# Kernel tuning notes

Hardware: AMD Instinct MI355X
Metric: run time of the kernel (lower is better)

Reference implementation:

```python
import jax, jax.numpy as jnp
import numpy as np

B, N, D, WIN = 2, 4096, 256, 16


def setup_inputs() -> dict:
    key = jax.random.key(0)
    ks = jax.random.split(key, 10)
    def lin(k, o, i):
        return 0.02 * jax.random.normal(k, (o, i), jnp.float32)
    W = N // WIN
    return {
        "x": 0.5 * jax.random.normal(ks[0], (B, N, D), jnp.float32),
        "embed_qk": jax.random.normal(ks[1], (3, B, W, WIN, WIN, 3), jnp.float32),
        "act_proj_w": lin(ks[2], D, D), "act_proj_b": jnp.zeros((D,), jnp.float32),
        "proj_ln_g": jnp.ones((D,), jnp.float32), "proj_ln_b": jnp.zeros((D,), jnp.float32),
        "conv_w": lin(ks[3], D, D), "conv_b": jnp.zeros((D,), jnp.float32),
        "q_w": lin(ks[4], D, D), "q_b": jnp.zeros((D,), jnp.float32),
        "k_w": lin(ks[5], D, D), "k_b": jnp.zeros((D,), jnp.float32),
        "p_w": lin(ks[6], 1, 3), "p_b": jnp.zeros((1,), jnp.float32),
        "lin_w": lin(ks[7], D, D), "lin_b": jnp.zeros((D,), jnp.float32),
        "norm_g": jnp.ones((D,), jnp.float32), "norm_b": jnp.zeros((D,), jnp.float32),
    }


def _ln(x, g, b, eps=1e-5):
    m = x.mean(-1, keepdims=True)
    v = ((x - m) ** 2).mean(-1, keepdims=True)
    return (x - m) * jax.lax.rsqrt(v + eps) * g + b


def reference(x, embed_qk, act_proj_w, act_proj_b, proj_ln_g, proj_ln_b,
              conv_w, conv_b, q_w, q_b, k_w, k_b, p_w, p_b,
              lin_w, lin_b, norm_g, norm_b):
    # MSMAttentionLayer: gated residual path
    act_res = jax.nn.silu(x @ act_proj_w.T + act_proj_b)          # (B,N,C)
    h = _ln(x, proj_ln_g, proj_ln_b)
    h = jax.nn.silu(h @ conv_w.T + conv_b)                        # 1x1 conv == per-token linear

    # MSMLMultiHeadAttention, stage=1 (window 4x4=16); N % 16 == 0 so add_row_num = 0
    q = jax.nn.elu(h @ q_w.T + q_b) + 1.0
    k = jax.nn.elu(h @ k_w.T + k_b) + 1.0
    v = h
    Bn, Nn, C = h.shape
    Wn = Nn // WIN
    q_win = q.reshape(Bn, Wn, WIN, C)
    k_win = k.reshape(Bn, Wn, WIN, C)
    v_win = v.reshape(Bn, Wn, WIN, C)
    # learned relative-position bias: Linear(3,1) on embed_qk[stage]
    p = (embed_qk[1] @ p_w.T + p_b)[..., 0]
    # second elu+1 feature map (applied on top of q/k which are already elu+1)
    phi_q = jax.nn.elu(q_win) + 1.0
    phi_k = jax.nn.elu(k_win) + 1.0
    # linear-attention style KV aggregation: reduces over windows w
    KV = jnp.einsum('bwmc,bwmd->bmcd', phi_k, v_win)
    att = jnp.einsum('bwnc,bmcd->bwnmd', phi_q, KV) + p[..., None]
    attn_out = att.reshape(Bn, -1, C)[:, :Nn, :]                  # (B,N,C)

    hid = (attn_out * act_res) @ lin_w.T + lin_b
    return _ln(hid + h, norm_g, norm_b)
```

## Files before the change

### kernel.cpp

```cpp
#include <hip/hip_runtime.h>


#define DIM 256
#define NTOK 4096

typedef __attribute__((ext_vector_type(8))) short short8;
typedef __attribute__((ext_vector_type(4))) short short4v;
typedef __attribute__((ext_vector_type(4))) float f32x4;

__device__ __forceinline__ float silu_f(float z) { return z / (1.f + __expf(-z)); }
__device__ __forceinline__ float elu2_f(float z) { return z > 0.f ? z + 2.f : __expf(z) + 1.f; }

__device__ __forceinline__ short f2bf(float f) {
    union { float f; unsigned u; } v; v.f = f;
    unsigned r = v.u + 0x7fffu + ((v.u >> 16) & 1u);
    return (short)(r >> 16);
}
__device__ __forceinline__ float bf2f(short s) {
    union { unsigned u; float f; } v; v.u = ((unsigned)(unsigned short)s) << 16;
    return v.f;
}
__device__ __forceinline__ short8 cvt8(const float* src) {
    const float4 a = *(const float4*)src;
    const float4 c = *(const float4*)(src + 4);
    short8 s;
    s[0] = f2bf(a.x); s[1] = f2bf(a.y); s[2] = f2bf(a.z); s[3] = f2bf(a.w);
    s[4] = f2bf(c.x); s[5] = f2bf(c.y); s[6] = f2bf(c.z); s[7] = f2bf(c.w);
    return s;
}
__device__ __forceinline__ void cast_chunk(const float* __restrict__ src, short* __restrict__ dst,
                                           int chunk, int tid) {
    const int base = chunk * 8192 + tid * 32;
    #pragma unroll
    for (int j = 0; j < 4; ++j)
        *(short8*)(dst + base + j * 8) = cvt8(src + base + j * 8);
}

__global__ __launch_bounds__(256) void fused_dual(
        const float* __restrict__ XF,
        const float* __restrict__ W0f, const float* __restrict__ b0, short* __restrict__ Y0,
        const float* __restrict__ W1f, const float* __restrict__ b1, short* __restrict__ Y1,
        const float* __restrict__ G, const float* __restrict__ Bt,
        const float* __restrict__ Wkf, short* __restrict__ WKB,
        const float* __restrict__ Wqf, short* __restrict__ WQB) {
    const int tid = threadIdx.x;
    if (blockIdx.x >= 64) {
        if (blockIdx.y == 0 && blockIdx.z == 0) {
            const int which = blockIdx.x - 64;
            if (which < 8) cast_chunk(Wkf, WKB, which, tid);
            else cast_chunk(Wqf, WQB, which - 8, tid);
        }
        return;
    }
    __shared__ __align__(16) short Xs[2][128 * 72];
    __shared__ __align__(16) short Ws[2][64 * 72];
    __shared__ float stats[128][2];
    const int zz = blockIdx.z;
    const float* Wf = zz ? W1f : W0f;
    const float* bias = zz ? b1 : b0;
    short* Y = zz ? Y1 : Y0;
    const int wv = tid >> 6, l = tid & 63;
    const int lr = l & 15, lk = l >> 4;
    const int r0 = blockIdx.x * 128, c0 = blockIdx.y * 64;
    const int wm = (wv >> 1) * 64, wn = (wv & 1) * 32;
    const int sr = tid >> 3, sc = (tid & 7) * 8;

    if (zz) {
        const int prow = tid >> 1, phalf = tid & 1;
        const float* src = XF + (size_t)(r0 + prow) * DIM + phalf * 128;
        float a1 = 0.f, a2 = 0.f;
        #pragma unroll 8
        for (int j = 0; j < 32; ++j) {
            const float4 v = *(const float4*)(src + j * 4);
            a1 += v.x + v.y + v.z + v.w;
            a2 += v.x * v.x + v.y * v.y + v.z * v.z + v.w * v.w;
        }
        a1 += __shfl_xor(a1, 1);
        a2 += __shfl_xor(a2, 1);
        if (!phalf) {
            const float mm = a1 * (1.f / DIM);
            stats[prow][0] = mm;
            stats[prow][1] = rsqrtf(a2 * (1.f / DIM) - mm * mm + 1e-5f);
        }
        __syncthreads();
    }

    f32x4 acc[4][2];
    #pragma unroll
    for (int i = 0; i < 4; ++i)
        #pragma unroll
        for (int j = 0; j < 2; ++j) acc[i][j] = (f32x4){0.f, 0.f, 0.f, 0.f};

    float4 xa[4][2], wa[2][2];
    #pragma unroll
    for (int p = 0; p < 4; ++p) {
        const float* src = XF + (size_t)(r0 + sr + p * 32) * DIM + sc;
        xa[p][0] = *(const float4*)src;
        xa[p][1] = *(const float4*)(src + 4);
    }
    #pragma unroll
    for (int p = 0; p < 2; ++p) {
        const float* src = Wf + (size_t)(c0 + sr + p * 32) * DIM + sc;
        wa[p][0] = *(const float4*)src;
        wa[p][1] = *(const float4*)(src + 4);
    }

    int buf = 0;
    for (int s = 0; s < 4; ++s) {
        const int kt = s * 64;
        if (zz) {
            const float4 g1 = *(const float4*)(G + kt + sc);
            const float4 g2 = *(const float4*)(G + kt + sc + 4);
            const float4 t1 = *(const float4*)(Bt + kt + sc);
            const float4 t2 = *(const float4*)(Bt + kt + sc + 4);
            const float gv[8] = {g1.x, g1.y, g1.z, g1.w, g2.x, g2.y, g2.z, g2.w};
            const float bv[8] = {t1.x, t1.y, t1.z, t1.w, t2.x, t2.y, t2.z, t2.w};
            #pragma unroll
            for (int p = 0; p < 4; ++p) {
                const int row = sr + p * 32;
                const float mm = stats[row][0], rs = stats[row][1];
                const float v[8] = {xa[p][0].x, xa[p][0].y, xa[p][0].z, xa[p][0].w,
                                    xa[p][1].x, xa[p][1].y, xa[p][1].z, xa[p][1].w};
                short8 sS;
                #pragma unroll
                for (int j = 0; j < 8; ++j) sS[j] = f2bf((v[j] - mm) * rs * gv[j] + bv[j]);
                *(short8*)&Xs[buf][row * 72 + sc] = sS;
            }
        } else {
            #pragma unroll
            for (int p = 0; p < 4; ++p) {
                const int row = sr + p * 32;
                const float v[8] = {xa[p][0].x, xa[p][0].y, xa[p][0].z, xa[p][0].w,
                                    xa[p][1].x, xa[p][1].y, xa[p][1].z, xa[p][1].w};
                short8 sS;
                #pragma unroll
                for (int j = 0; j < 8; ++j) sS[j] = f2bf(v[j]);
                *(short8*)&Xs[buf][row * 72 + sc] = sS;
            }
        }
        #pragma unroll
        for (int p = 0; p < 2; ++p) {
            const int row = sr + p * 32;
            const float v[8] = {wa[p][0].x, wa[p][0].y, wa[p][0].z, wa[p][0].w,
                                wa[p][1].x, wa[p][1].y, wa[p][1].z, wa[p][1].w};
            short8 sS;
            #pragma unroll
            for (int j = 0; j < 8; ++j) sS[j] = f2bf(v[j]);
            *(short8*)&Ws[buf][row * 72 + sc] = sS;
        }
        __syncthreads();
        if (s < 3) {
            const int ktn = kt + 64;
            #pragma unroll
            for (int p = 0; p < 4; ++p) {
                const float* src = XF + (size_t)(r0 + sr + p * 32) * DIM + ktn + sc;
                xa[p][0] = *(const float4*)src;
                xa[p][1] = *(const float4*)(src + 4);
            }
            #pragma unroll
            for (int p = 0; p < 2; ++p) {
                const float* src = Wf + (size_t)(c0 + sr + p * 32) * DIM + ktn + sc;
                wa[p][0] = *(const float4*)src;
                wa[p][1] = *(const float4*)(src + 4);
            }
        }
        #pragma unroll
        for (int kc = 0; kc < 2; ++kc) {
            short8 af[4], bfr[2];
            #pragma unroll
            for (int mi = 0; mi < 4; ++mi)
                af[mi] = *(const short8*)&Xs[buf][(wm + mi * 16 + lr) * 72 + kc * 32 + lk * 8];
            #pragma unroll
            for (int ni = 0; ni < 2; ++ni)
                bfr[ni] = *(const short8*)&Ws[buf][(wn + ni * 16 + lr) * 72 + kc * 32 + lk * 8];
            #pragma unroll
            for (int mi = 0; mi < 4; ++mi)
                #pragma unroll
                for (int ni = 0; ni < 2; ++ni)
                    acc[mi][ni] = __builtin_amdgcn_mfma_f32_16x16x32_bf16(af[mi], bfr[ni], acc[mi][ni], 0, 0, 0);
        }
        buf ^= 1;
    }
    #pragma unroll
    for (int mi = 0; mi < 4; ++mi)
        #pragma unroll
        for (int ni = 0; ni < 2; ++ni) {
            const int c = c0 + wn + ni * 16 + lr;
            const float bv2 = bias[c];
            #pragma unroll
            for (int i = 0; i < 4; ++i) {
                const int r = r0 + wm + mi * 16 + lk * 4 + i;
                Y[(size_t)r * DIM + c] = f2bf(silu_f(acc[mi][ni][i] + bv2));
            }
        }
}

__global__ __launch_bounds__(256) void gemm_kq(
        const short* __restrict__ H, const short* __restrict__ WKB, const float* __restrict__ bk, short* __restrict__ PK,
        const short* __restrict__ WQB, const float* __restrict__ bq, short* __restrict__ PQ) {
    __shared__ __align__(16) short Xs[2][128 * 72];
    __shared__ __align__(16) short Ws[2][64 * 72];
    const int bx = blockIdx.x;
    const bool isq = bx >= 64;
    const short* W = isq ? WQB : WKB;
    const float* bias = isq ? bq : bk;
    short* Y = isq ? PQ : PK;
    const int r0 = (isq ? bx - 64 : bx) * 128;
    const int c0 = blockIdx.y * 64;
    const int tid = threadIdx.x;
    const int wv = tid >> 6, l = tid & 63;
    const int lr = l & 15, lk = l >> 4;
    const int wm = (wv >> 1) * 64, wn = (wv & 1) * 32;
    const int sr = tid >> 3, sc = (tid & 7) * 8;

    int growA[4];
    #pragma unroll
    for (int p = 0; p < 4; ++p) {
        int grow = r0 + sr + p * 32;
        if (isq) grow = ((grow >> 8) << 12) + (grow & 255);
        growA[p] = grow;
    }

    f32x4 acc[4][2];
    #pragma unroll
    for (int i = 0; i < 4; ++i)
        #pragma unroll
        for (int j = 0; j < 2; ++j) acc[i][j] = (f32x4){0.f, 0.f, 0.f, 0.f};

    short8 xa[4], wa[2];
    #pragma unroll
    for (int p = 0; p < 4; ++p)
        xa[p] = *(const short8*)(H + (size_t)growA[p] * DIM + sc);
    #pragma unroll
    for (int p = 0; p < 2; ++p)
        wa[p] = *(const short8*)(W + (size_t)(c0 + sr + p * 32) * DIM + sc);

    int buf = 0;
    for (int s = 0; s < 4; ++s) {
        #pragma unroll
        for (int p = 0; p < 4; ++p)
            *(short8*)&Xs[buf][(sr + p * 32) * 72 + sc] = xa[p];
        #pragma unroll
        for (int p = 0; p < 2; ++p)
            *(short8*)&Ws[buf][(sr + p * 32) * 72 + sc] = wa[p];
        __syncthreads();
        if (s < 3) {
            const int ktn = (s + 1) * 64;
            #pragma unroll
            for (int p = 0; p < 4; ++p)
                xa[p] = *(const short8*)(H + (size_t)growA[p] * DIM + ktn + sc);
            #pragma unroll
            for (int p = 0; p < 2; ++p)
                wa[p] = *(const short8*)(W + (size_t)(c0 + sr + p * 32) * DIM + ktn + sc);
        }
        #pragma unroll
        for (int kc = 0; kc < 2; ++kc) {
            short8 af[4], bfr[2];
            #pragma unroll
            for (int mi = 0; mi < 4; ++mi)
                af[mi] = *(const short8*)&Xs[buf][(wm + mi * 16 + lr) * 72 + kc * 32 + lk * 8];
            #pragma unroll
            for (int ni = 0; ni < 2; ++ni)
                bfr[ni] = *(const short8*)&Ws[buf][(wn + ni * 16 + lr) * 72 + kc * 32 + lk * 8];
            #pragma unroll
            for (int mi = 0; mi < 4; ++mi)
                #pragma unroll
                for (int ni = 0; ni < 2; ++ni)
                    acc[mi][ni] = __builtin_amdgcn_mfma_f32_16x16x32_bf16(af[mi], bfr[ni], acc[mi][ni], 0, 0, 0);
        }
        buf ^= 1;
    }
    #pragma unroll
    for (int mi = 0; mi < 4; ++mi)
        #pragma unroll
        for (int ni = 0; ni < 2; ++ni) {
            const int c = c0 + wn + ni * 16 + lr;
            const float bv = bias[c];
            #pragma unroll
            for (int i = 0; i < 4; ++i) {
                const int r = r0 + wm + mi * 16 + lk * 4 + i;
                Y[(size_t)r * DIM + c] = f2bf(elu2_f(acc[mi][ni][i] + bv));
            }
        }
}

__global__ __launch_bounds__(256) void kv_mfma(const short* __restrict__ HB, const short* __restrict__ PK,
                                               short* __restrict__ KVT,
                                               const float* __restrict__ Wlf, short* __restrict__ WLB) {
    const int tid = threadIdx.x;
    if (blockIdx.x >= 32) {
        if (blockIdx.y == 0 && blockIdx.z == 0)
            cast_chunk(Wlf, WLB, blockIdx.x - 32, tid);
        return;
    }
    __shared__ __align__(16) short Hs[64 * 68];
    __shared__ __align__(16) short Ps[64 * 68];
    const int bm = blockIdx.x, b = bm >> 4, m = bm & 15;
    const int d0 = blockIdx.y * 64, c0 = blockIdx.z * 64;
    const int wv = tid >> 6, l = tid & 63;
    const int lr = l & 15, lk = l >> 4;
    const int wd = (wv >> 1) * 32, wc = (wv & 1) * 32;
    f32x4 acc[2][2];
    #pragma unroll
    for (int i = 0; i < 2; ++i)
        #pragma unroll
        for (int j = 0; j < 2; ++j) acc[i][j] = (f32x4){0.f, 0.f, 0.f, 0.f};
    const size_t hbase = (size_t)b * NTOK * DIM;
    const int sr = tid >> 3, sc = (tid & 7) * 8;
    for (int kt = 0; kt < 256; kt += 64) {
        #pragma unroll
        for (int p = 0; p < 2; ++p) {
            const int w = sr + p * 32;
            const size_t gg = hbase + (size_t)((kt + w) * 16 + m) * DIM;
            short8 hv = *(const short8*)(HB + gg + d0 + sc);
            short8 pv = *(const short8*)(PK + gg + c0 + sc);
            *(short4v*)&Hs[w * 68 + sc]     = __builtin_shufflevector(hv, hv, 0, 1, 2, 3);
            *(short4v*)&Hs[w * 68 + sc + 4] = __builtin_shufflevector(hv, hv, 4, 5, 6, 7);
            *(short4v*)&Ps[w * 68 + sc]     = __builtin_shufflevector(pv, pv, 0, 1, 2, 3);
            *(short4v*)&Ps[w * 68 + sc + 4] = __builtin_shufflevector(pv, pv, 4, 5, 6, 7);
        }
        __syncthreads();
        #pragma unroll
        for (int kc = 0; kc < 2; ++kc) {
            const int kb = kc * 32 + lk * 8;
            short8 af[2], bfr[2];
            #pragma unroll
            for (int di = 0; di < 2; ++di)
                #pragma unroll
                for (int i = 0; i < 8; ++i)
                    af[di][i] = Hs[(kb + i) * 68 + wd + di * 16 + lr];
            #pragma unroll
            for (int ci = 0; ci < 2; ++ci)
                #pragma unroll
                for (int i = 0; i < 8; ++i)
                    bfr[ci][i] = Ps[(kb + i) * 68 + wc + ci * 16 + lr];
            #pragma unroll
            for (int di = 0; di < 2; ++di)
                #pragma unroll
                for (int ci = 0; ci < 2; ++ci)
                    acc[di][ci] = __builtin_amdgcn_mfma_f32_16x16x32_bf16(af[di], bfr[ci], acc[di][ci], 0, 0, 0);
        }
        __syncthreads();
    }
    #pragma unroll
    for (int di = 0; di < 2; ++di)
        #pragma unroll
        for (int ci = 0; ci < 2; ++ci)
            #pragma unroll
            for (int i = 0; i < 4; ++i) {
                const int d = d0 + wd + di * 16 + lk * 4 + i;
                const int c = c0 + wc + ci * 16 + lr;
                KVT[((size_t)bm * DIM + d) * DIM + c] = f2bf(acc[di][ci][i]);
            }
}

__global__ __launch_bounds__(256) void attlin(
        const short* __restrict__ PQ, const short* __restrict__ KVT,
        const float* __restrict__ emb, const float* __restrict__ pw, const float* __restrict__ pb,
        const short* __restrict__ AR,
        const short* __restrict__ WLB, const float* __restrict__ bl,
        const short* __restrict__ HB, const float* __restrict__ G, const float* __restrict__ Bt,
        float* __restrict__ Y) {
    __shared__ __align__(16) short Qs[32 * 264];
    __shared__ __align__(16) short AGs[32 * 264];
    __shared__ __align__(16) short Bs[256 * 72];
    __shared__ float s1buf[32][2];
    __shared__ float s2buf[32][2];
    const int tid = threadIdx.x;
    const int wv = tid >> 6, l = tid & 63;
    const int lr = l & 15, lk = l >> 4;
    const int bm = blockIdx.x, b = bm >> 4, m = bm & 15;
    const int q0 = blockIdx.y * 32;
    const int wq = (wv >> 1) * 16;
    const int wd = (wv & 1) * 32;
    const int sr = tid >> 3, sc = (tid & 7) * 8;

    #pragma unroll
    for (int p = 0; p < 4; ++p) {
        const int chunk = tid + p * 256;
        const int row = chunk >> 5, cc = (chunk & 31) * 8;
        *(short8*)&Qs[row * 264 + cc] = *(const short8*)(PQ + (size_t)(b * 256 + q0 + row) * DIM + cc);
    }

    f32x4 accA[4][2];
    #pragma unroll
    for (int i = 0; i < 4; ++i)
        #pragma unroll
        for (int j = 0; j < 2; ++j) accA[i][j] = (f32x4){0.f, 0.f, 0.f, 0.f};
    for (int kt = 0; kt < DIM; kt += 64) {
        #pragma unroll
        for (int p = 0; p < 8; ++p) {
            const int row = sr + p * 32;
            *(short8*)&Bs[row * 72 + sc] = *(const short8*)(KVT + ((size_t)bm * DIM + row) * DIM + kt + sc);
        }
        __syncthreads();
        #pragma unroll
        for (int kc = 0; kc < 2; ++kc) {
            const short8 af = *(const short8*)&Qs[(wq + lr) * 264 + kt + kc * 32 + lk * 8];
            #pragma unroll
            for (int dc = 0; dc < 4; ++dc)
                #pragma unroll
                for (int ni = 0; ni < 2; ++ni) {
                    const short8 bfr = *(const short8*)&Bs[(dc * 64 + wd + ni * 16 + lr) * 72 + kc * 32 + lk * 8];
                    accA[dc][ni] = __builtin_amdgcn_mfma_f32_16x16x32_bf16(af, bfr, accA[dc][ni], 0, 0, 0);
                }
        }
        __syncthreads();
    }
    {
        const float pw0 = pw[0], pw1 = pw[1], pw2 = pw[2], pbv = pb[0];
        #pragma unroll
        for (int i = 0; i < 4; ++i) {
            const int rloc = wq + lk * 4 + i;
            const int qr = q0 + rloc;
            const int widx = qr >> 4, nidx = qr & 15;
            const float* e = emb + ((((size_t)(2 + b) * 256 + widx) * 16 + nidx) * 16 + m) * 3;
            const float pv = e[0] * pw0 + e[1] * pw1 + e[2] * pw2 + pbv;
            const int t = qr * 16 + m;
            #pragma unroll
            for (int dc = 0; dc < 4; ++dc)
                #pragma unroll
                for (int ni = 0; ni < 2; ++ni) {
                    const int d = dc * 64 + wd + ni * 16 + lr;
                    const size_t o = ((size_t)b * NTOK + t) * DIM + d;
                    AGs[rloc * 264 + d] = f2bf((accA[dc][ni][i] + pv) * bf2f(AR[o]));
                }
        }
    }
    __syncthreads();

    const int wn2 = (wv & 1) * 128;
    f32x4 accB[8];
    #pragma unroll
    for (int i = 0; i < 8; ++i) accB[i] = (f32x4){0.f, 0.f, 0.f, 0.f};
    for (int kt = 0; kt < DIM; kt += 64) {
        #pragma unroll
        for (int p = 0; p < 8; ++p) {
            const int row = sr + p * 32;
            *(short8*)&Bs[row * 72 + sc] = *(const short8*)(WLB + (size_t)row * DIM + kt + sc);
        }
        __syncthreads();
        #pragma unroll
        for (int kc = 0; kc < 2; ++kc) {
            const short8 af = *(const short8*)&AGs[(wq + lr) * 264 + kt + kc * 32 + lk * 8];
            #pragma unroll
            for (int ni = 0; ni < 8; ++ni) {
                const short8 bfr = *(const short8*)&Bs[(wn2 + ni * 16 + lr) * 72 + kc * 32 + lk * 8];
                accB[ni] = __builtin_amdgcn_mfma_f32_16x16x32_bf16(af, bfr, accB[ni], 0, 0, 0);
            }
        }
        __syncthreads();
    }
    float s1[4] = {0.f, 0.f, 0.f, 0.f}, s2[4] = {0.f, 0.f, 0.f, 0.f};
    #pragma unroll
    for (int ni = 0; ni < 8; ++ni) {
        const int col = wn2 + ni * 16 + lr;
        const float bv = bl[col];
        #pragma unroll
        for (int i = 0; i < 4; ++i) {
            const int rloc = wq + lk * 4 + i;
            const int t = (q0 + rloc) * 16 + m;
            const float z = accB[ni][i] + bv + bf2f(HB[((size_t)b * NTOK + t) * DIM + col]);
            accB[ni][i] = z;
            s1[i] += z; s2[i] += z * z;
        }
    }
    #pragma unroll
    for (int o = 1; o < 16; o <<= 1) {
        #pragma unroll
        for (int i = 0; i < 4; ++i) {
            s1[i] += __shfl_xor(s1[i], o);
            s2[i] += __shfl_xor(s2[i], o);
        }
    }
    if (lr == 0) {
        #pragma unroll
        for (int i = 0; i < 4; ++i) {
            const int rloc = wq + lk * 4 + i;
            s1buf[rloc][wv & 1] = s1[i];
            s2buf[rloc][wv & 1] = s2[i];
        }
    }
    __syncthreads();
    float mean[4], rstd[4];
    #pragma unroll
    for (int i = 0; i < 4; ++i) {
        const int rloc = wq + lk * 4 + i;
        const float t1 = s1buf[rloc][0] + s1buf[rloc][1];
        const float t2 = s2buf[rloc][0] + s2buf[rloc][1];
        const float mm = t1 * (1.f / DIM);
        mean[i] = mm;
        rstd[i] = rsqrtf(t2 * (1.f / DIM) - mm * mm + 1e-5f);
    }
    #pragma unroll
    for (int ni = 0; ni < 8; ++ni) {
        const int col = wn2 + ni * 16 + lr;
        const float gv = G[col], bv2 = Bt[col];
        #pragma unroll
        for (int i = 0; i < 4; ++i) {
            const int rloc = wq + lk * 4 + i;
            const int t = (q0 + rloc) * 16 + m;
            Y[((size_t)b * NTOK + t) * DIM + col] = (accB[ni][i] - mean[i]) * rstd[i] * gv + bv2;
        }
    }
}

extern "C" void kernel_launch(void* const* d_in, const int* in_sizes, int n_in,
                              void* d_out, int out_size, void* d_ws, size_t ws_size,
                              hipStream_t stream) {
    const float* x   = (const float*)d_in[0];
    const float* emb = (const float*)d_in[1];
    const float* Wa  = (const float*)d_in[2];
    const float* ba  = (const float*)d_in[3];
    const float* lng = (const float*)d_in[4];
    const float* lnb = (const float*)d_in[5];
    const float* Wc  = (const float*)d_in[6];
    const float* bc  = (const float*)d_in[7];
    const float* Wq  = (const float*)d_in[8];
    const float* bq  = (const float*)d_in[9];
    const float* Wk  = (const float*)d_in[10];
    const float* bk  = (const float*)d_in[11];
    const float* pw  = (const float*)d_in[12];
    const float* pb  = (const float*)d_in[13];
    const float* Wl  = (const float*)d_in[14];
    const float* bl  = (const float*)d_in[15];
    const float* ng  = (const float*)d_in[16];
    const float* nb  = (const float*)d_in[17];

    char* ws = (char*)d_ws;
    const size_t MB = 1024 * 1024;
    short* h_bf   = (short*)(ws + 0 * MB);
    short* phik   = (short*)(ws + 4 * MB);
    short* phiq   = (short*)(ws + 8 * MB);
    short* kvT    = (short*)(ws + 9 * MB);
    short* act_bf = (short*)(ws + 13 * MB);
    short* Wk_bf  = (short*)(ws + 17 * MB);
    short* Wq_bf  = (short*)(ws + 17 * MB + 128 * 1024);
    short* Wl_bf  = (short*)(ws + 17 * MB + 256 * 1024);

    fused_dual<<<dim3(80, 4, 2), dim3(256), 0, stream>>>(x, Wa, ba, act_bf,
                                                         Wc, bc, h_bf, lng, lnb,
                                                         Wk, Wk_bf, Wq, Wq_bf);
    gemm_kq<<<dim3(68, 4), dim3(256), 0, stream>>>(h_bf, Wk_bf, bk, phik, Wq_bf, bq, phiq);
    kv_mfma<<<dim3(40, 4, 4), dim3(256), 0, stream>>>(h_bf, phik, kvT, Wl, Wl_bf);
    attlin<<<dim3(32, 8), dim3(256), 0, stream>>>(phiq, kvT, emb, pw, pb, act_bf, Wl_bf, bl,
                                                  h_bf, ng, nb, (float*)d_out);
}
```

Baseline: 53.86 us.

## Double-buffer LDS tiles with register prefetch in kv and attention GEMM loops

Converts the K-loops in kv_mfma and both GEMM phases of attlin to double-buffered shared memory. The next tile is prefetched into registers while MFMAs run on the current buffer, which also drops one barrier per iteration. The aim is to hide global load latency behind compute. In exchange, LDS use doubles (attlin's Bs grows to about 72KB), which may lower occupancy, and more registers are live during the loop.

```diff
diff --git a/kernel.cpp b/kernel.cpp
--- a/kernel.cpp
+++ b/kernel.cpp
@@ -293,8 +293,8 @@
             cast_chunk(Wlf, WLB, blockIdx.x - 32, tid);
         return;
     }
-    __shared__ __align__(16) short Hs[64 * 68];
-    __shared__ __align__(16) short Ps[64 * 68];
+    __shared__ __align__(16) short Hs[2][64 * 68];
+    __shared__ __align__(16) short Ps[2][64 * 68];
     const int bm = blockIdx.x, b = bm >> 4, m = bm & 15;
     const int d0 = blockIdx.y * 64, c0 = blockIdx.z * 64;
     const int wv = tid >> 6, l = tid & 63;
@@ -307,19 +307,37 @@
         for (int j = 0; j < 2; ++j) acc[i][j] = (f32x4){0.f, 0.f, 0.f, 0.f};
     const size_t hbase = (size_t)b * NTOK * DIM;
     const int sr = tid >> 3, sc = (tid & 7) * 8;
-    for (int kt = 0; kt < 256; kt += 64) {
+
+    short8 hv[2], pv[2];
+    #pragma unroll
+    for (int p = 0; p < 2; ++p) {
+        const int w = sr + p * 32;
+        const size_t gg = hbase + (size_t)(w * 16 + m) * DIM;
+        hv[p] = *(const short8*)(HB + gg + d0 + sc);
+        pv[p] = *(const short8*)(PK + gg + c0 + sc);
+    }
+
+    int buf = 0;
+    for (int s = 0; s < 4; ++s) {
         #pragma unroll
         for (int p = 0; p < 2; ++p) {
             const int w = sr + p * 32;
-            const size_t gg = hbase + (size_t)((kt + w) * 16 + m) * DIM;
-            short8 hv = *(const short8*)(HB + gg + d0 + sc);
-            short8 pv = *(const short8*)(PK + gg + c0 + sc);
-            *(short4v*)&Hs[w * 68 + sc]     = __builtin_shufflevector(hv, hv, 0, 1, 2, 3);
-            *(short4v*)&Hs[w * 68 + sc + 4] = __builtin_shufflevector(hv, hv, 4, 5, 6, 7);
-            *(short4v*)&Ps[w * 68 + sc]     = __builtin_shufflevector(pv, pv, 0, 1, 2, 3);
-            *(short4v*)&Ps[w * 68 + sc + 4] = __builtin_shufflevector(pv, pv, 4, 5, 6, 7);
+            *(short4v*)&Hs[buf][w * 68 + sc]     = __builtin_shufflevector(hv[p], hv[p], 0, 1, 2, 3);
+            *(short4v*)&Hs[buf][w * 68 + sc + 4] = __builtin_shufflevector(hv[p], hv[p], 4, 5, 6, 7);
+            *(short4v*)&Ps[buf][w * 68 + sc]     = __builtin_shufflevector(pv[p], pv[p], 0, 1, 2, 3);
+            *(short4v*)&Ps[buf][w * 68 + sc + 4] = __builtin_shufflevector(pv[p], pv[p], 4, 5, 6, 7);
         }
         __syncthreads();
+        if (s < 3) {
+            const int ktn = (s + 1) * 64;
+            #pragma unroll
+            for (int p = 0; p < 2; ++p) {
+                const int w = sr + p * 32;
+                const size_t gg = hbase + (size_t)((ktn + w) * 16 + m) * DIM;
+                hv[p] = *(const short8*)(HB + gg + d0 + sc);
+                pv[p] = *(const short8*)(PK + gg + c0 + sc);
+            }
+        }
         #pragma unroll
         for (int kc = 0; kc < 2; ++kc) {
             const int kb = kc * 32 + lk * 8;
@@ -328,19 +346,19 @@
             for (int di = 0; di < 2; ++di)
                 #pragma unroll
                 for (int i = 0; i < 8; ++i)
-                    af[di][i] = Hs[(kb + i) * 68 + wd + di * 16 + lr];
+                    af[di][i] = Hs[buf][(kb + i) * 68 + wd + di * 16 + lr];
             #pragma unroll
             for (int ci = 0; ci < 2; ++ci)
                 #pragma unroll
                 for (int i = 0; i < 8; ++i)
-                    bfr[ci][i] = Ps[(kb + i) * 68 + wc + ci * 16 + lr];
+                    bfr[ci][i] = Ps[buf][(kb + i) * 68 + wc + ci * 16 + lr];
             #pragma unroll
             for (int di = 0; di < 2; ++di)
                 #pragma unroll
                 for (int ci = 0; ci < 2; ++ci)
                     acc[di][ci] = __builtin_amdgcn_mfma_f32_16x16x32_bf16(af[di], bfr[ci], acc[di][ci], 0, 0, 0);
         }
-        __syncthreads();
+        buf ^= 1;
     }
     #pragma unroll
     for (int di = 0; di < 2; ++di)
@@ -363,7 +381,7 @@
         float* __restrict__ Y) {
     __shared__ __align__(16) short Qs[32 * 264];
     __shared__ __align__(16) short AGs[32 * 264];
-    __shared__ __align__(16) short Bs[256 * 72];
+    __shared__ __align__(16) short Bs[2][256 * 72];
     __shared__ float s1buf[32][2];
     __shared__ float s2buf[32][2];
     const int tid = threadIdx.x;
@@ -387,13 +405,23 @@
     for (int i = 0; i < 4; ++i)
         #pragma unroll
         for (int j = 0; j < 2; ++j) accA[i][j] = (f32x4){0.f, 0.f, 0.f, 0.f};
-    for (int kt = 0; kt < DIM; kt += 64) {
-        #pragma unroll
-        for (int p = 0; p < 8; ++p) {
-            const int row = sr + p * 32;
-            *(short8*)&Bs[row * 72 + sc] = *(const short8*)(KVT + ((size_t)bm * DIM + row) * DIM + kt + sc);
-        }
+    short8 bv8[8];
+    #pragma unroll
+    for (int p = 0; p < 8; ++p)
+        bv8[p] = *(const short8*)(KVT + ((size_t)bm * DIM + sr + p * 32) * DIM + sc);
+    int buf = 0;
+    for (int s = 0; s < 4; ++s) {
+        const int kt = s * 64;
+        #pragma unroll
+        for (int p = 0; p < 8; ++p)
+            *(short8*)&Bs[buf][(sr + p * 32) * 72 + sc] = bv8[p];
         __syncthreads();
+        if (s < 3) {
+            const int ktn = kt + 64;
+            #pragma unroll
+            for (int p = 0; p < 8; ++p)
+                bv8[p] = *(const short8*)(KVT + ((size_t)bm * DIM + sr + p * 32) * DIM + ktn + sc);
+        }
         #pragma unroll
         for (int kc = 0; kc < 2; ++kc) {
             const short8 af = *(const short8*)&Qs[(wq + lr) * 264 + kt + kc * 32 + lk * 8];
@@ -401,12 +429,13 @@
             for (int dc = 0; dc < 4; ++dc)
                 #pragma unroll
                 for (int ni = 0; ni < 2; ++ni) {
-                    const short8 bfr = *(const short8*)&Bs[(dc * 64 + wd + ni * 16 + lr) * 72 + kc * 32 + lk * 8];
+                    const short8 bfr = *(const short8*)&Bs[buf][(dc * 64 + wd + ni * 16 + lr) * 72 + kc * 32 + lk * 8];
                     accA[dc][ni] = __builtin_amdgcn_mfma_f32_16x16x32_bf16(af, bfr, accA[dc][ni], 0, 0, 0);
                 }
         }
-        __syncthreads();
-    }
+        buf ^= 1;
+    }
+    __syncthreads();
     {
         const float pw0 = pw[0], pw1 = pw[1], pw2 = pw[2], pbv = pb[0];
         #pragma unroll
@@ -433,23 +462,32 @@
     f32x4 accB[8];
     #pragma unroll
     for (int i = 0; i < 8; ++i) accB[i] = (f32x4){0.f, 0.f, 0.f, 0.f};
-    for (int kt = 0; kt < DIM; kt += 64) {
-        #pragma unroll
-        for (int p = 0; p < 8; ++p) {
-            const int row = sr + p * 32;
-            *(short8*)&Bs[row * 72 + sc] = *(const short8*)(WLB + (size_t)row * DIM + kt + sc);
-        }
+    #pragma unroll
+    for (int p = 0; p < 8; ++p)
+        bv8[p] = *(const short8*)(WLB + (size_t)(sr + p * 32) * DIM + sc);
+    buf = 0;
+    for (int s = 0; s < 4; ++s) {
+        const int kt = s * 64;
+        #pragma unroll
+        for (int p = 0; p < 8; ++p)
+            *(short8*)&Bs[buf][(sr + p * 32) * 72 + sc] = bv8[p];
         __syncthreads();
+        if (s < 3) {
+            const int ktn = kt + 64;
+            #pragma unroll
+            for (int p = 0; p < 8; ++p)
+                bv8[p] = *(const short8*)(WLB + (size_t)(sr + p * 32) * DIM + ktn + sc);
+        }
         #pragma unroll
         for (int kc = 0; kc < 2; ++kc) {
             const short8 af = *(const short8*)&AGs[(wq + lr) * 264 + kt + kc * 32 + lk * 8];
             #pragma unroll
             for (int ni = 0; ni < 8; ++ni) {
-                const short8 bfr = *(const short8*)&Bs[(wn2 + ni * 16 + lr) * 72 + kc * 32 + lk * 8];
+                const short8 bfr = *(const short8*)&Bs[buf][(wn2 + ni * 16 + lr) * 72 + kc * 32 + lk * 8];
                 accB[ni] = __builtin_amdgcn_mfma_f32_16x16x32_bf16(af, bfr, accB[ni], 0, 0, 0);
             }
         }
-        __syncthreads();
+        buf ^= 1;
     }
     float s1[4] = {0.f, 0.f, 0.f, 0.f}, s2[4] = {0.f, 0.f, 0.f, 0.f};
     #pragma unroll
```

Result: no change. 53.39 us, median of 2 (-0.9%).
